# Kernel optimization log

Measured on AMD Instinct MI355X. Metric: run time of the kernel, lower is better.

## Reference

```python
import jax, jax.numpy as jnp
import numpy as np

H = 256            # hidden_dim
E = H // 2         # uniform_dim = 128
NH = 4             # num_heads
DH = E // NH       # head_dim = 32
OUT = 256          # output_dim
B = 65536
LN_EPS = 1e-5


def _lin(k, din, dout):
    kw, kb = jax.random.split(k)
    bound = 1.0 / np.sqrt(din)
    W = jax.random.uniform(kw, (din, dout), jnp.float32, -bound, bound)
    b = jax.random.uniform(kb, (dout,), jnp.float32, -bound, bound)
    return W, b


def setup_inputs() -> dict:
    key = jax.random.key(0)
    ks = jax.random.split(key, 20)
    x = jax.random.normal(ks[0], (B, 29), jnp.float32)
    # component encoders (Linear + ReLU)
    Wv, bv = _lin(ks[1], 3, H // 4)
    Wm, bm = _lin(ks[2], 5, H // 4)
    Wi, bi = _lin(ks[3], 2, H // 8)
    Wb, bb = _lin(ks[4], 3, H // 8)
    Wc, bc = _lin(ks[5], 6, H // 4)
    Wf, bf = _lin(ks[6], 10, H // 2)
    # projections to uniform_dim
    Pv, pv = _lin(ks[7], H // 4, E)
    Pm, pm = _lin(ks[8], H // 4, E)
    Pi, pi = _lin(ks[9], H // 8, E)
    Pb, pb = _lin(ks[10], H // 8, E)
    Pc, pc = _lin(ks[11], H // 4, E)
    Pf, pf = _lin(ks[12], H // 2, E)
    # multi-head attention (packed QKV in_proj + out_proj), stored as [in,out]
    Wqkv, bqkv = _lin(ks[13], E, 3 * E)
    Wo, bo = _lin(ks[14], E, E)
    # layernorm
    g = jnp.ones((E,), jnp.float32)
    beta = jnp.zeros((E,), jnp.float32)
    # pool projection
    Wp, bp = _lin(ks[15], E, OUT)
    return dict(x=x, Wv=Wv, bv=bv, Wm=Wm, bm=bm, Wi=Wi, bi=bi, Wb=Wb, bb=bb,
                Wc=Wc, bc=bc, Wf=Wf, bf=bf, Pv=Pv, pv=pv, Pm=Pm, pm=pm,
                Pi=Pi, pi=pi, Pb=Pb, pb=pb, Pc=Pc, pc=pc, Pf=Pf, pf=pf,
                Wqkv=Wqkv, bqkv=bqkv, Wo=Wo, bo=bo, g=g, beta=beta, Wp=Wp, bp=bp)


def _forward(x, Wv, bv, Wm, bm, Wi, bi, Wb, bb, Wc, bc, Wf, bf,
             Pv, pv, Pm, pm, Pi, pi, Pb, pb, Pc, pc, Pf, pf,
             Wqkv, bqkv, Wo, bo, g, beta, Wp, bp):
    enc = lambda v, W, b: jax.nn.relu(v @ W + b)
    # component encoders + projections -> 6 tokens of dim E
    t_v = enc(x[:, 0:3], Wv, bv) @ Pv + pv
    t_m = enc(x[:, 3:8], Wm, bm) @ Pm + pm
    t_i = enc(x[:, 8:10], Wi, bi) @ Pi + pi
    t_b = enc(x[:, 10:13], Wb, bb) @ Pb + pb
    t_c = enc(x[:, 13:19], Wc, bc) @ Pc + pc
    t_f = enc(x[:, 19:29], Wf, bf) @ Pf + pf
    tokens = jnp.stack([t_v, t_m, t_i, t_b, t_c, t_f], axis=1)  # [B,6,E]
    Bn = tokens.shape[0]
    # self-attention (torch MultiheadAttention, batch_first, eval mode)
    qkv = tokens @ Wqkv + bqkv                                   # [B,6,3E]
    q, k, v = jnp.split(qkv, 3, axis=-1)
    q = q.reshape(Bn, 6, NH, DH)
    k = k.reshape(Bn, 6, NH, DH)
    v = v.reshape(Bn, 6, NH, DH)
    scores = jnp.einsum('bqhd,bkhd->bhqk', q, k) / np.sqrt(DH)  # [B,H,6,6]
    attn = jax.nn.softmax(scores, axis=-1)
    ctx = jnp.einsum('bhqk,bkhd->bqhd', attn, v).reshape(Bn, 6, E)
    attn_out = ctx @ Wo + bo
    # residual + layernorm
    h = tokens + attn_out
    mu = jnp.mean(h, axis=-1, keepdims=True)
    var = jnp.mean(jnp.square(h - mu), axis=-1, keepdims=True)
    h = (h - mu) * jax.lax.rsqrt(var + LN_EPS) * g + beta
    # mean-pool over 6 tokens, project, relu
    pooled = jnp.mean(h, axis=1)                                 # [B,E]
    return jax.nn.relu(pooled @ Wp + bp)                         # [B,OUT]


def reference(x, Wv, bv, Wm, bm, Wi, bi, Wb, bb, Wc, bc, Wf, bf,
              Pv, pv, Pm, pm, Pi, pi, Pb, pb, Pc, pc, Pf, pf,
              Wqkv, bqkv, Wo, bo, g, beta, Wp, bp):
    return _forward(x, Wv, bv, Wm, bm, Wi, bi, Wb, bb, Wc, bc, Wf, bf,
                    Pv, pv, Pm, pm, Pi, pi, Pb, pb, Pc, pc, Pf, pf,
                    Wqkv, bqkv, Wo, bo, g, beta, Wp, bp)
```

## Files before the change

### kernel.cpp

```cpp
#include <hip/hip_runtime.h>
#include <math.h>

typedef float f32x4 __attribute__((ext_vector_type(4)));
typedef short short8 __attribute__((ext_vector_type(8)));
typedef unsigned short u16;

#define LN_EPS 1e-5f

static __device__ __forceinline__ unsigned cvt_pk_bf16(float lo, float hi) {
    unsigned r;
    asm("v_cvt_pk_bf16_f32 %0, %1, %2" : "=v"(r) : "v"(lo), "v"(hi));
    return r;
}
static __device__ __forceinline__ u16 f2bf(float f) { return (u16)cvt_pk_bf16(f, f); }
static __device__ __forceinline__ float bf2f(u16 u) {
    return __uint_as_float(((unsigned)u) << 16);
}

#define OFF_QKV 0
#define OFF_WO  49152
#define OFF_WP  65536
#define OFF_PV  98304
#define OFF_PM  106496
#define OFF_PI  114688
#define OFF_PB  118784
#define OFF_PC  122880
#define OFF_PF  131072
#define OFF_WENC 147456
#define OFF_BENC 172032
#define CW_TOTAL 172416

__global__ __launch_bounds__(512) void convert_weights(
    const float* __restrict__ Wqkv, const float* __restrict__ Wo, const float* __restrict__ Wp,
    const float* __restrict__ Pv, const float* __restrict__ Pm, const float* __restrict__ Pi,
    const float* __restrict__ Pb, const float* __restrict__ Pc, const float* __restrict__ Pf,
    const float* __restrict__ Wv, const float* __restrict__ Wm, const float* __restrict__ Wi,
    const float* __restrict__ Wb, const float* __restrict__ Wc, const float* __restrict__ Wf,
    const float* __restrict__ bv, const float* __restrict__ bm, const float* __restrict__ bi,
    const float* __restrict__ bb, const float* __restrict__ bc, const float* __restrict__ bf_,
    u16* __restrict__ ws)
{
    int gid = blockIdx.x * 512 + threadIdx.x;
    if (gid < OFF_WENC) {
        const float* src; int N, Ksteps, local;
        if (gid < OFF_WO)      { src = Wqkv; N = 384; Ksteps = 4; local = gid; }
        else if (gid < OFF_WP) { src = Wo;   N = 128; Ksteps = 4; local = gid - OFF_WO; }
        else if (gid < OFF_PV) { src = Wp;   N = 256; Ksteps = 4; local = gid - OFF_WP; }
        else if (gid < OFF_PM) { src = Pv;   N = 128; Ksteps = 2; local = gid - OFF_PV; }
        else if (gid < OFF_PI) { src = Pm;   N = 128; Ksteps = 2; local = gid - OFF_PM; }
        else if (gid < OFF_PB) { src = Pi;   N = 128; Ksteps = 1; local = gid - OFF_PI; }
        else if (gid < OFF_PC) { src = Pb;   N = 128; Ksteps = 1; local = gid - OFF_PB; }
        else if (gid < OFF_PF) { src = Pc;   N = 128; Ksteps = 2; local = gid - OFF_PC; }
        else                   { src = Pf;   N = 128; Ksteps = 4; local = gid - OFF_PF; }
        int j  = local & 7;
        int l  = (local >> 3) & 63;
        int r2 = local >> 9;
        int kk = r2 % Ksteps;
        int nt = r2 / Ksteps;
        int srow = kk * 32 + (l >> 4) * 8 + j;
        int scol = nt * 16 + (l & 15);
        ws[gid] = f2bf(src[srow * N + scol]);
    } else if (gid < OFF_BENC) {
        int local = gid - OFF_WENC;
        int j = local & 7, l = (local >> 3) & 63, r2 = local >> 9;
        int kk = r2 & 1, nt = r2 >> 1;
        int k = kk * 32 + (l >> 4) * 8 + j;
        int r = k & 31;
        int scol = nt * 16 + (l & 15);
        const float* W; int cb, xo, din, dout;
        if (scol < 64)       { W = Wv; cb = 0;   xo = 0;  din = 3;  dout = 64; }
        else if (scol < 128) { W = Wm; cb = 64;  xo = 3;  din = 5;  dout = 64; }
        else if (scol < 160) { W = Wi; cb = 128; xo = 8;  din = 2;  dout = 32; }
        else if (scol < 192) { W = Wb; cb = 160; xo = 10; din = 3;  dout = 32; }
        else if (scol < 256) { W = Wc; cb = 192; xo = 13; din = 6;  dout = 64; }
        else                 { W = Wf; cb = 256; xo = 19; din = 10; dout = 128; }
        int rr = r - xo;
        float val = (r < 29 && rr >= 0 && rr < din) ? W[rr * dout + (scol - cb)] : 0.f;
        ws[gid] = f2bf(val);
    } else if (gid < CW_TOTAL) {
        int j = gid - OFF_BENC;
        const float* b; int off;
        if (j < 64)       { b = bv;  off = 0; }
        else if (j < 128) { b = bm;  off = 64; }
        else if (j < 160) { b = bi;  off = 128; }
        else if (j < 192) { b = bb;  off = 160; }
        else if (j < 256) { b = bc;  off = 192; }
        else              { b = bf_; off = 256; }
        ((float*)(ws + OFF_BENC))[j] = b[j - off];
    }
}

__global__ __launch_bounds__(512, 4) void asmlp_mfma(
    const float* __restrict__ x,
    const float* __restrict__ pv, const float* __restrict__ pm,
    const float* __restrict__ pi_, const float* __restrict__ pb_,
    const float* __restrict__ pc_, const float* __restrict__ pf_,
    const float* __restrict__ bqkv, const float* __restrict__ bo,
    const float* __restrict__ gg, const float* __restrict__ beta,
    const float* __restrict__ bp,
    const u16* __restrict__ ws,
    float* __restrict__ out)
{
    const int blk  = blockIdx.x;
    const int t    = threadIdx.x;
    const int lane = t & 63;
    const int wv   = t >> 6;
    const int col  = lane & 15;
    const int lg   = lane >> 4;

    __shared__ __attribute__((aligned(16))) u16 sm[26624];
    u16*   s_tok  = sm;
    u16*   s_qk   = sm + 6144;
    u16*   s_vt   = sm + 18432;
    u16*   s_xa   = sm + 18432;
    u16*   s_h    = sm + 18944;
    u16*   s_ctx  = sm + 6144;
    u16*   s_pp   = sm + 12288;
    float* s_out  = (float*)(sm + 12288);
    u16*   s_pool = sm + 18432;

    if (t < 232) {
        int row = t / 29, cc = t - row * 29;
        float f = x[(size_t)blk * 232 + t];
        u16 hi = f2bf(f);
        float lo = f - bf2f(hi);
        s_xa[row * 64 + (((cc >> 3) ^ (row & 3)) << 3) + (cc & 7)] = hi;
        int c2 = cc + 32;
        s_xa[row * 64 + (((c2 >> 3) ^ (row & 3)) << 3) + (c2 & 7)] = f2bf(lo);
    }
    if (t < 48) {
        int row = t / 6, sl = t - (t / 6) * 6;
        int k = (sl < 3) ? (29 + sl) : (58 + sl);
        s_xa[row * 64 + (((k >> 3) ^ (row & 3)) << 3) + (k & 7)] = 0;
    }
    __syncthreads();

    {
        int row8 = col & 7;
        short8 B0 = *(const short8*)&s_xa[row8 * 64 + ((lg ^ (row8 & 3)) << 3)];
        short8 B1 = *(const short8*)&s_xa[row8 * 64 + (((4 + lg) ^ (row8 & 3)) << 3)];
        const float* benc = (const float*)(ws + OFF_BENC);
        #pragma unroll
        for (int q = 0; q < 3; ++q) {
            int nt = wv * 3 + q;
            f32x4 acc = *(const f32x4*)&benc[nt * 16 + lg * 4];
            short8 A0 = *(const short8*)&ws[OFF_WENC + (((nt * 2 + 0) * 64 + lane) << 3)];
            short8 A1 = *(const short8*)&ws[OFF_WENC + (((nt * 2 + 1) * 64 + lane) << 3)];
            acc = __builtin_amdgcn_mfma_f32_16x16x32_bf16(A0, B0, acc, 0, 0, 0);
            acc = __builtin_amdgcn_mfma_f32_16x16x32_bf16(A1, B1, acc, 0, 0, 0);
            if (col < 8) {
                int ge = nt * 2 + (lg >> 1);
                uint2 w;
                w.x = cvt_pk_bf16(fmaxf(acc[0], 0.f), fmaxf(acc[1], 0.f));
                w.y = cvt_pk_bf16(fmaxf(acc[2], 0.f), fmaxf(acc[3], 0.f));
                *(uint2*)&s_h[((col * 48 + (ge ^ col)) << 3) + (lg & 1) * 4] = w;
            }
        }
    }
    __syncthreads();

    #pragma unroll
    for (int q = 0; q < 6; ++q) {
        int unit = wv * 6 + q;
        int c = unit >> 3, n = unit & 7;
        const float* bias; int ks, hg, wso;
        switch (c) {
            case 0:  bias = pv;  ks = 2; hg = 0;  wso = OFF_PV; break;
            case 1:  bias = pm;  ks = 2; hg = 8;  wso = OFF_PM; break;
            case 2:  bias = pi_; ks = 1; hg = 16; wso = OFF_PI; break;
            case 3:  bias = pb_; ks = 1; hg = 20; wso = OFF_PB; break;
            case 4:  bias = pc_; ks = 2; hg = 24; wso = OFF_PC; break;
            default: bias = pf_; ks = 4; hg = 32; wso = OFF_PF; break;
        }
        f32x4 acc = *(const f32x4*)&bias[n * 16 + lg * 4];
        int hrow = col & 7;
        for (int kk = 0; kk < ks; ++kk) {
            short8 A = *(const short8*)&ws[wso + (((n * ks + kk) * 64 + lane) << 3)];
            short8 B = *(const short8*)&s_h[(hrow * 48 + ((hg + kk * 4 + lg) ^ hrow)) << 3];
            acc = __builtin_amdgcn_mfma_f32_16x16x32_bf16(A, B, acc, 0, 0, 0);
        }
        if (col < 8) {
            int tok = c * 8 + col;
            int gt = n * 2 + (lg >> 1);
            uint2 w;
            w.x = cvt_pk_bf16(acc[0], acc[1]);
            w.y = cvt_pk_bf16(acc[2], acc[3]);
            *(uint2*)&s_tok[((tok * 16 + (gt ^ (tok & 15))) << 3) + (lg & 1) * 4] = w;
        }
    }
    __syncthreads();

    {
        short8 Bf[3][4];
        float  bb_[3];
        #pragma unroll
        for (int ni = 0; ni < 3; ++ni) {
            int n = wv * 3 + ni;
            bb_[ni] = bqkv[n * 16 + col];
            #pragma unroll
            for (int kk = 0; kk < 4; ++kk)
                Bf[ni][kk] = *(const short8*)&ws[OFF_QKV + (((n * 4 + kk) * 64 + lane) << 3)];
        }
        { uint2 z; z.x = 0u; z.y = 0u; *(uint2*)&s_vt[t * 16 + 12] = z; }
        for (int mt = 0; mt < 3; ++mt) {
            short8 A[4];
            int arow = mt * 16 + col;
            #pragma unroll
            for (int kk = 0; kk < 4; ++kk) {
                int g = kk * 4 + lg;
                A[kk] = *(const short8*)&s_tok[(arow * 16 + (g ^ (arow & 15))) << 3];
            }
            #pragma unroll
            for (int ni = 0; ni < 3; ++ni) {
                f32x4 acc = {bb_[ni], bb_[ni], bb_[ni], bb_[ni]};
                #pragma unroll
                for (int kk = 0; kk < 4; ++kk)
                    acc = __builtin_amdgcn_mfma_f32_16x16x32_bf16(A[kk], Bf[ni][kk], acc, 0, 0, 0);
                int cn = wv * 3 + ni;
                int cg = cn * 16 + col;
                if (cn < 16) {
                    int q4 = ((cg >> 3) & 3) << 2;
                    int tb = (mt * 16 + lg * 4) ^ q4;
                    uint2 w;
                    w.x = cvt_pk_bf16(acc[0], acc[1]);
                    w.y = cvt_pk_bf16(acc[2], acc[3]);
                    *(uint2*)&s_qk[cg * 48 + tb] = w;
                } else {
                    int d = cg - 256;
                    int h = d >> 5, ch = (d >> 4) & 1, nn = d & 15;
                    #pragma unroll
                    for (int r = 0; r < 4; ++r) {
                        int token = mt * 16 + lg * 4 + r;
                        int c2 = token >> 3, rb = token & 7;
                        int g2 = rb * 2 + (h >> 1);
                        int kidx = (h & 1) * 6 + c2;
                        s_vt[((g2 * 2 + ch) * 16 + nn) * 16 + kidx] = f2bf(acc[r]);
                    }
                }
            }
        }
    }
    __syncthreads();

    f32x4 scf[2];
    {
        const int rb = wv;
        #pragma unroll
        for (int i = 0; i < 2; ++i) {
            const int hp = i;
            int p  = (col >= 6 && col < 12) ? 1 : 0;
            int qi = (col < 6) ? col : ((col < 12) ? col - 6 : 0);
            int tt = qi * 8 + rb;
            int h  = hp * 2 + p;
            int tsw = tt ^ (lg << 2);
            int abase = (h * 32 + lg * 8) * 48 + tsw;
            int bbase = (128 + h * 32 + lg * 8) * 48 + tsw;
            short8 Aq, Bk;
            #pragma unroll
            for (int j = 0; j < 8; ++j) {
                Aq[j] = (short)s_qk[abase + j * 48];
                Bk[j] = (short)s_qk[bbase + j * 48];
            }
            f32x4 sc = {0.f, 0.f, 0.f, 0.f};
            scf[i] = __builtin_amdgcn_mfma_f32_16x16x32_bf16(Aq, Bk, sc, 0, 0, 0);
        }
    }
    __syncthreads();

    {
        #pragma unroll
        for (int i = 0; i < 2; ++i) {
            u16* pp = s_pp + (wv * 2 + i) * 256;
            f32x4 pr4;
            #pragma unroll
            for (int r = 0; r < 4; ++r) {
                int mr = lg * 4 + r;
                int prr = (mr >= 6 && mr < 12) ? 1 : 0;
                float v = scf[i][r] * 0.17677669529663687f;
                bool inR = (col >= 6 * prr) && (col < 6 * prr + 6);
                float mv = inR ? v : -1e30f;
                #pragma unroll
                for (int off = 1; off < 16; off <<= 1)
                    mv = fmaxf(mv, __shfl_xor(mv, off, 16));
                float e = inR ? __expf(v - mv) : 0.f;
                float s = e;
                #pragma unroll
                for (int off = 1; off < 16; off <<= 1)
                    s += __shfl_xor(s, off, 16);
                pr4[r] = (mr < 12) ? (e / s) : 0.f;
            }
            uint2 w;
            w.x = cvt_pk_bf16(pr4[0], pr4[1]);
            w.y = cvt_pk_bf16(pr4[2], pr4[3]);
            *(uint2*)&pp[col * 16 + lg * 4] = w;
        }
    }
    __syncthreads();

    {
        const int rb = wv;
        #pragma unroll
        for (int i = 0; i < 2; ++i) {
            const int hp = i;
            u16* pp = s_pp + (wv * 2 + i) * 256;
            short8 Ap;
            if (lg < 2) {
                #pragma unroll
                for (int j = 0; j < 8; ++j)
                    Ap[j] = (short)pp[(lg * 8 + j) * 16 + col];
            } else {
                #pragma unroll
                for (int j = 0; j < 8; ++j) Ap[j] = 0;
            }
            int g2 = rb * 2 + hp;
            #pragma unroll
            for (int ch = 0; ch < 2; ++ch) {
                short8 Bv = *(const short8*)&s_vt[(((g2 * 2 + ch) * 16 + col) * 16) + ((lg & 1) * 8)];
                f32x4 c = {0.f, 0.f, 0.f, 0.f};
                c = __builtin_amdgcn_mfma_f32_16x16x32_bf16(Ap, Bv, c, 0, 0, 0);
                #pragma unroll
                for (int r = 0; r < 4; ++r) {
                    int mr = lg * 4 + r;
                    if (mr < 12) {
                        int pq = mr >= 6 ? 1 : 0;
                        int qi = mr - 6 * pq;
                        int token = qi * 8 + rb;
                        int d = (hp * 2 + pq) * 32 + ch * 16 + col;
                        s_ctx[((token * 16 + ((d >> 3) ^ (token & 15))) << 3) + (d & 7)] = f2bf(c[r]);
                    }
                }
            }
        }
    }
    __syncthreads();

    if (wv < 3) {
        int mt = wv;
        int arow = mt * 16 + col;
        short8 A[4];
        #pragma unroll
        for (int kk = 0; kk < 4; ++kk) {
            int g = kk * 4 + lg;
            A[kk] = *(const short8*)&s_ctx[(arow * 16 + (g ^ (arow & 15))) << 3];
        }
        f32x4 acc[8];
        #pragma unroll
        for (int n = 0; n < 8; ++n) {
            float b = bo[n * 16 + col];
            acc[n] = (f32x4){b, b, b, b};
            #pragma unroll
            for (int kk = 0; kk < 4; ++kk) {
                short8 Bf = *(const short8*)&ws[OFF_WO + (((n * 4 + kk) * 64 + lane) << 3)];
                acc[n] = __builtin_amdgcn_mfma_f32_16x16x32_bf16(A[kk], Bf, acc[n], 0, 0, 0);
            }
        }
        #pragma unroll
        for (int n = 0; n < 8; ++n) {
            int cn = n * 16 + col;
            #pragma unroll
            for (int r = 0; r < 4; ++r) {
                int row = mt * 16 + lg * 4 + r;
                acc[n][r] += bf2f(s_tok[((row * 16 + ((cn >> 3) ^ (row & 15))) << 3) + (cn & 7)]);
            }
        }
        float mu_[4], rs_[4];
        #pragma unroll
        for (int r = 0; r < 4; ++r) {
            float s1 = 0.f, s2 = 0.f;
            #pragma unroll
            for (int n = 0; n < 8; ++n) { float v = acc[n][r]; s1 += v; s2 += v * v; }
            #pragma unroll
            for (int off = 1; off <= 8; off <<= 1) {
                s1 += __shfl_xor(s1, off, 64);
                s2 += __shfl_xor(s2, off, 64);
            }
            float mu  = s1 * (1.f / 128.f);
            float var = s2 * (1.f / 128.f) - mu * mu;
            mu_[r] = mu;
            rs_[r] = rsqrtf(var + LN_EPS);
        }
        #pragma unroll
        for (int n = 0; n < 8; ++n) {
            int cn = n * 16 + col;
            float gw = gg[cn], bw = beta[cn];
            #pragma unroll
            for (int r = 0; r < 4; ++r) {
                int row = mt * 16 + lg * 4 + r;
                float val = (acc[n][r] - mu_[r]) * rs_[r] * gw + bw;
                s_tok[((row * 16 + ((cn >> 3) ^ (row & 15))) << 3) + (cn & 7)] = f2bf(val);
            }
        }
    }
    __syncthreads();

    if (t < 128) {
        int row = t >> 4, gch = t & 15;
        float fa[8] = {0, 0, 0, 0, 0, 0, 0, 0};
        #pragma unroll
        for (int c = 0; c < 6; ++c) {
            int tok = c * 8 + row;
            short8 v = *(const short8*)&s_tok[(tok * 16 + (gch ^ (tok & 15))) << 3];
            #pragma unroll
            for (int j = 0; j < 8; ++j) fa[j] += bf2f((u16)v[j]);
        }
        short8 o;
        #pragma unroll
        for (int j = 0; j < 8; ++j) o[j] = (short)f2bf(fa[j] * (1.f / 6.f));
        *(short8*)&s_pool[(row * 16 + (gch ^ row)) << 3] = o;
    }
    __syncthreads();

    {
        int arow = col & 7;
        short8 A[4];
        #pragma unroll
        for (int kk = 0; kk < 4; ++kk) {
            int g = kk * 4 + lg;
            A[kk] = *(const short8*)&s_pool[(arow * 16 + (g ^ arow)) << 3];
        }
        #pragma unroll
        for (int ni = 0; ni < 2; ++ni) {
            int n = wv * 2 + ni;
            float b = bp[n * 16 + col];
            f32x4 acc = {b, b, b, b};
            #pragma unroll
            for (int kk = 0; kk < 4; ++kk) {
                short8 Bf = *(const short8*)&ws[OFF_WP + (((n * 4 + kk) * 64 + lane) << 3)];
                acc = __builtin_amdgcn_mfma_f32_16x16x32_bf16(A[kk], Bf, acc, 0, 0, 0);
            }
            if (lg < 2) {
                #pragma unroll
                for (int r = 0; r < 4; ++r) {
                    int row = lg * 4 + r;
                    s_out[row * 260 + n * 16 + col] = fmaxf(acc[r], 0.f);
                }
            }
        }
    }
    __syncthreads();

    if (t < 256) {
        int row = t >> 5, c8 = (t & 31) * 8;
        f32x4 v0 = *(const f32x4*)&s_out[row * 260 + c8];
        f32x4 v1 = *(const f32x4*)&s_out[row * 260 + c8 + 4];
        float* dst = out + ((size_t)blk * 8 + row) * 256 + c8;
        *(f32x4*)dst = v0;
        *(f32x4*)(dst + 4) = v1;
    }
}

extern "C" void kernel_launch(void* const* d_in, const int* in_sizes, int n_in,
                              void* d_out, int out_size, void* d_ws, size_t ws_size,
                              hipStream_t stream) {
    const float* x    = (const float*)d_in[0];
    const float* Wv   = (const float*)d_in[1];
    const float* bv   = (const float*)d_in[2];
    const float* Wm   = (const float*)d_in[3];
    const float* bm   = (const float*)d_in[4];
    const float* Wi   = (const float*)d_in[5];
    const float* bi   = (const float*)d_in[6];
    const float* Wb   = (const float*)d_in[7];
    const float* bb   = (const float*)d_in[8];
    const float* Wc   = (const float*)d_in[9];
    const float* bc   = (const float*)d_in[10];
    const float* Wf   = (const float*)d_in[11];
    const float* bf_  = (const float*)d_in[12];
    const float* Pv   = (const float*)d_in[13];
    const float* pv   = (const float*)d_in[14];
    const float* Pm   = (const float*)d_in[15];
    const float* pm   = (const float*)d_in[16];
    const float* Pi   = (const float*)d_in[17];
    const float* pii  = (const float*)d_in[18];
    const float* Pb   = (const float*)d_in[19];
    const float* pb   = (const float*)d_in[20];
    const float* Pc   = (const float*)d_in[21];
    const float* pc   = (const float*)d_in[22];
    const float* Pf   = (const float*)d_in[23];
    const float* pf   = (const float*)d_in[24];
    const float* Wqkv = (const float*)d_in[25];
    const float* bqkv = (const float*)d_in[26];
    const float* Wo   = (const float*)d_in[27];
    const float* bo   = (const float*)d_in[28];
    const float* gg   = (const float*)d_in[29];
    const float* beta = (const float*)d_in[30];
    const float* Wp   = (const float*)d_in[31];
    const float* bp   = (const float*)d_in[32];
    float* out = (float*)d_out;
    u16* ws = (u16*)d_ws;

    convert_weights<<<(CW_TOTAL + 511) / 512, 512, 0, stream>>>(
        Wqkv, Wo, Wp, Pv, Pm, Pi, Pb, Pc, Pf,
        Wv, Wm, Wi, Wb, Wc, Wf, bv, bm, bi, bb, bc, bf_, ws);

    const int Bn = in_sizes[0] / 29;
    asmlp_mfma<<<Bn / 8, 512, 0, stream>>>(
        x, pv, pm, pii, pb, pc, pf,
        bqkv, bo, gg, beta, bp, ws, out);
}
```

Baseline: 294.2 us.

## Split out-projection and LayerNorm across all 8 waves by output columns

The out-projection plus residual-and-LayerNorm stage used to run on only 3 waves, one per 16-token row tile, each covering all 128 output columns. It now runs on all 8 waves, each owning 16 output columns for every token, with Wo acting as the A operand and the context as B. Per-token LayerNorm sums are reduced through a shared-memory partial buffer, which needs an extra __syncthreads. Stores are packed as bf16 pairs. The aim is to remove idle waves in this stage, at the cost of more LDS traffic and one more barrier.

```diff
diff --git a/kernel.cpp b/kernel.cpp
--- a/kernel.cpp
+++ b/kernel.cpp
@@ -116,6 +116,7 @@
     u16*   s_h    = sm + 18944;
     u16*   s_ctx  = sm + 6144;
     u16*   s_pp   = sm + 12288;
+    float* s_part = (float*)(sm + 12288);
     float* s_out  = (float*)(sm + 12288);
     u16*   s_pool = sm + 18432;
 
@@ -334,61 +335,57 @@
     }
     __syncthreads();
 
-    if (wv < 3) {
-        int mt = wv;
-        int arow = mt * 16 + col;
-        short8 A[4];
-        #pragma unroll
-        for (int kk = 0; kk < 4; ++kk) {
-            int g = kk * 4 + lg;
-            A[kk] = *(const short8*)&s_ctx[(arow * 16 + (g ^ (arow & 15))) << 3];
-        }
-        f32x4 acc[8];
-        #pragma unroll
-        for (int n = 0; n < 8; ++n) {
-            float b = bo[n * 16 + col];
-            acc[n] = (f32x4){b, b, b, b};
+    {
+        const int mo = wv;
+        short8 Afr[4];
+        #pragma unroll
+        for (int kk = 0; kk < 4; ++kk)
+            Afr[kk] = *(const short8*)&ws[OFF_WO + (((mo * 4 + kk) * 64 + lane) << 3)];
+        f32x4 biasv = *(const f32x4*)&bo[mo * 16 + lg * 4];
+        f32x4 accs[3];
+        #pragma unroll
+        for (int tt = 0; tt < 3; ++tt) {
+            int tokr = tt * 16 + col;
+            f32x4 acc = biasv;
             #pragma unroll
             for (int kk = 0; kk < 4; ++kk) {
-                short8 Bf = *(const short8*)&ws[OFF_WO + (((n * 4 + kk) * 64 + lane) << 3)];
-                acc[n] = __builtin_amdgcn_mfma_f32_16x16x32_bf16(A[kk], Bf, acc[n], 0, 0, 0);
-            }
-        }
-        #pragma unroll
-        for (int n = 0; n < 8; ++n) {
-            int cn = n * 16 + col;
-            #pragma unroll
-            for (int r = 0; r < 4; ++r) {
-                int row = mt * 16 + lg * 4 + r;
-                acc[n][r] += bf2f(s_tok[((row * 16 + ((cn >> 3) ^ (row & 15))) << 3) + (cn & 7)]);
-            }
-        }
-        float mu_[4], rs_[4];
-        #pragma unroll
-        for (int r = 0; r < 4; ++r) {
-            float s1 = 0.f, s2 = 0.f;
-            #pragma unroll
-            for (int n = 0; n < 8; ++n) { float v = acc[n][r]; s1 += v; s2 += v * v; }
-            #pragma unroll
-            for (int off = 1; off <= 8; off <<= 1) {
-                s1 += __shfl_xor(s1, off, 64);
-                s2 += __shfl_xor(s2, off, 64);
-            }
-            float mu  = s1 * (1.f / 128.f);
-            float var = s2 * (1.f / 128.f) - mu * mu;
-            mu_[r] = mu;
-            rs_[r] = rsqrtf(var + LN_EPS);
-        }
-        #pragma unroll
-        for (int n = 0; n < 8; ++n) {
-            int cn = n * 16 + col;
-            float gw = gg[cn], bw = beta[cn];
-            #pragma unroll
-            for (int r = 0; r < 4; ++r) {
-                int row = mt * 16 + lg * 4 + r;
-                float val = (acc[n][r] - mu_[r]) * rs_[r] * gw + bw;
-                s_tok[((row * 16 + ((cn >> 3) ^ (row & 15))) << 3) + (cn & 7)] = f2bf(val);
-            }
+                short8 Bf = *(const short8*)&s_ctx[(tokr * 16 + ((kk * 4 + lg) ^ (tokr & 15))) << 3];
+                acc = __builtin_amdgcn_mfma_f32_16x16x32_bf16(Afr[kk], Bf, acc, 0, 0, 0);
+            }
+            const u16* rp = &s_tok[((tokr * 16 + ((mo * 2 + (lg >> 1)) ^ (tokr & 15))) << 3) + (lg & 1) * 4];
+            #pragma unroll
+            for (int r = 0; r < 4; ++r) acc[r] += bf2f(rp[r]);
+            accs[tt] = acc;
+            float s1 = acc[0] + acc[1] + acc[2] + acc[3];
+            float s2 = acc[0]*acc[0] + acc[1]*acc[1] + acc[2]*acc[2] + acc[3]*acc[3];
+            s1 += __shfl_xor(s1, 16, 64); s1 += __shfl_xor(s1, 32, 64);
+            s2 += __shfl_xor(s2, 16, 64); s2 += __shfl_xor(s2, 32, 64);
+            if (lg == 0) {
+                float2 pw; pw.x = s1; pw.y = s2;
+                *(float2*)&s_part[(tokr * 8 + wv) * 2] = pw;
+            }
+        }
+        __syncthreads();
+        f32x4 gv = *(const f32x4*)&gg[mo * 16 + lg * 4];
+        f32x4 bv = *(const f32x4*)&beta[mo * 16 + lg * 4];
+        #pragma unroll
+        for (int tt = 0; tt < 3; ++tt) {
+            int tokr = tt * 16 + col;
+            const float* pr = &s_part[tokr * 16];
+            f32x4 p0 = *(const f32x4*)pr;
+            f32x4 p1 = *(const f32x4*)(pr + 4);
+            f32x4 p2 = *(const f32x4*)(pr + 8);
+            f32x4 p3 = *(const f32x4*)(pr + 12);
+            float S1 = p0[0]+p0[2]+p1[0]+p1[2]+p2[0]+p2[2]+p3[0]+p3[2];
+            float S2 = p0[1]+p0[3]+p1[1]+p1[3]+p2[1]+p2[3]+p3[1]+p3[3];
+            float mu = S1 * (1.f / 128.f);
+            float var = S2 * (1.f / 128.f) - mu * mu;
+            float rs = rsqrtf(var + LN_EPS);
+            f32x4 a = accs[tt];
+            uint2 w;
+            w.x = cvt_pk_bf16((a[0]-mu)*rs*gv[0]+bv[0], (a[1]-mu)*rs*gv[1]+bv[1]);
+            w.y = cvt_pk_bf16((a[2]-mu)*rs*gv[2]+bv[2], (a[3]-mu)*rs*gv[3]+bv[3]);
+            *(uint2*)&s_tok[((tokr * 16 + ((mo * 2 + (lg >> 1)) ^ (tokr & 15))) << 3) + (lg & 1) * 4] = w;
         }
     }
     __syncthreads();
```

New measurement: 288.0 us. -2.1%, faster.
